# Optimization experiments

Hardware: AMD Instinct MI355X
Metric: run time of the kernel (lower is better)

## Reference

```python
import jax, jax.numpy as jnp
import numpy as np

B, T, I, H, A = 128, 1024, 128, 256, 40


def setup_inputs() -> dict:
    key = jax.random.key(0)
    ks = jax.random.split(key, 10)
    s_ih = 1.0 / np.sqrt(H)
    return {
        "x": jax.random.normal(ks[0], (B, T, I), dtype=jnp.float32),
        "W_ih": jax.random.uniform(ks[1], (3 * H, I), minval=-s_ih, maxval=s_ih, dtype=jnp.float32),
        "W_hh": jax.random.uniform(ks[2], (3 * H, H), minval=-s_ih, maxval=s_ih, dtype=jnp.float32),
        "b_ih": jax.random.uniform(ks[3], (3 * H,), minval=-s_ih, maxval=s_ih, dtype=jnp.float32),
        "b_hh": jax.random.uniform(ks[4], (3 * H,), minval=-s_ih, maxval=s_ih, dtype=jnp.float32),
        "wv_W": jax.random.normal(ks[5], (A, H), dtype=jnp.float32) * 0.05,
        "wv_b": jnp.zeros((A,), dtype=jnp.float32),
        "wu": jax.random.uniform(ks[6], (A,), dtype=jnp.float32),
        "h2o_W": jax.random.normal(ks[7], (1, H), dtype=jnp.float32) * 0.05,
        "h2o_b": jnp.zeros((1,), dtype=jnp.float32),
    }


def _gru_outputs(x, W_ih, W_hh, b_ih, b_hh):
    # Precompute input-side gate projections for all timesteps: [B,T,3H]
    gx = jnp.einsum("bti,gi->btg", x, W_ih) + b_ih
    h0 = jnp.zeros((x.shape[0], H), dtype=x.dtype)

    def step(h, gx_t):
        gh = h @ W_hh.T + b_hh                      # [B,3H]
        xr, xz, xn = jnp.split(gx_t, 3, axis=-1)    # torch gate order r,z,n
        hr, hz, hn = jnp.split(gh, 3, axis=-1)
        r = jax.nn.sigmoid(xr + hr)
        z = jax.nn.sigmoid(xz + hz)
        n = jnp.tanh(xn + r * hn)
        h_new = (1.0 - z) * n + z * h
        return h_new, h_new

    _, hs = jax.lax.scan(step, h0, jnp.swapaxes(gx, 0, 1))  # hs: [T,B,H]
    return jnp.swapaxes(hs, 0, 1)  # [B,T,H]


def reference(x, W_ih, W_hh, b_ih, b_hh, wv_W, wv_b, wu, h2o_W, h2o_b):
    outputs = _gru_outputs(x, W_ih, W_hh, b_ih, b_hh)          # [B,T,H]
    um = jnp.tanh(jnp.einsum("bth,ah->bta", outputs, wv_W) + wv_b)  # [B,T,A]
    alpha = jax.nn.softmax(um @ wu, axis=1)                    # [B,T]
    context = jnp.einsum("bt,bth->bh", alpha, outputs)         # [B,H]
    # dropout_layer is identity in eval mode
    out = context @ h2o_W.T + h2o_b                            # [B,1]
    return out
```

## Files before the change

### kernel.cpp

```cpp
#include <hip/hip_runtime.h>


#define B_ 128
#define T_ 1024
#define I_ 128
#define H_ 256
#define G_ 768
#define A_ 40

typedef _Float16 f16;
typedef _Float16 f16x2 __attribute__((ext_vector_type(2)));
typedef _Float16 f16x8 __attribute__((ext_vector_type(8)));
typedef float    f32x4 __attribute__((ext_vector_type(4)));

__device__ __forceinline__ float fdot2(unsigned a, unsigned b, float c){
#if __has_builtin(__builtin_amdgcn_fdot2)
  return __builtin_amdgcn_fdot2(__builtin_bit_cast(f16x2, a),
                                __builtin_bit_cast(f16x2, b), c, false);
#else
  f16x2 av = __builtin_bit_cast(f16x2, a), bv = __builtin_bit_cast(f16x2, b);
  return c + (float)av.x * (float)bv.x + (float)av.y * (float)bv.y;
#endif
}

__device__ __forceinline__ float2 h2f(unsigned u){
  f16x2 h = __builtin_bit_cast(f16x2, u);
  return make_float2((float)h.x, (float)h.y);
}
__device__ __forceinline__ unsigned f2h2(float a, float b){
  f16x2 h; h.x = (f16)a; h.y = (f16)b;
  return __builtin_bit_cast(unsigned, h);
}
__device__ __forceinline__ float rcp_(float x){ return __builtin_amdgcn_rcpf(x); }
__device__ __forceinline__ float sigm_(float x){ return rcp_(1.f + __expf(-x)); }
__device__ __forceinline__ float tanh_(float x){ return 1.f - 2.f * rcp_(__expf(2.f * x) + 1.f); }

__device__ __forceinline__ float pl16_sum(float x){
  float y = x;
  asm volatile("v_permlane16_swap_b32 %0, %1" : "+v"(x), "+v"(y));
  return x + y;
}
__device__ __forceinline__ float pl32_sum(float x){
  float y = x;
  asm volatile("v_permlane32_swap_b32 %0, %1" : "+v"(x), "+v"(y));
  return x + y;
}

__global__ __launch_bounds__(256) void k_prep_w(const float* __restrict__ W,
                                                unsigned* __restrict__ Wp){
  int idx = blockIdx.x * 256 + threadIdx.x;
  int dd  = idx >> 10;
  int col = idx & 1023;
  int c = dd >> 5, d = dd & 31;
  int rt = ((col >> 6) << 4) | (col & 15);
  int qs = (col >> 4) & 3;
  int r = c * 256 + rt;
  int k = qs * 64 + 2 * d;
  Wp[(size_t)dd * 1024 + col] = f2h2(W[r * 256 + k], W[r * 256 + k + 1]);
}

__global__ __launch_bounds__(256) void k_gx(const float* __restrict__ x,
                                            const float* __restrict__ wih,
                                            const float* __restrict__ bih,
                                            const float* __restrict__ bhh,
                                            f16* __restrict__ gx){
  __shared__ __align__(16) f16 XA[128 * 128];
  __shared__ __align__(16) f16 XB[64 * 128];
  const int tid = threadIdx.x;
  const int m0 = blockIdx.x * 128, n0 = blockIdx.y * 64;

  #pragma unroll
  for (int u = 0; u < 16; ++u){
    int idx = tid + 256 * u;
    int row = idx >> 5, k4 = idx & 31;
    float4 v = *(const float4*)(x + (size_t)(m0 + row) * I_ + k4 * 4);
    unsigned byte = (unsigned)(row * 256 + k4 * 8) ^ ((row & 7) << 4);
    *(uint2*)((char*)XA + byte) = make_uint2(f2h2(v.x, v.y), f2h2(v.z, v.w));
  }
  #pragma unroll
  for (int u = 0; u < 8; ++u){
    int idx = tid + 256 * u;
    int row = idx >> 5, k4 = idx & 31;
    float4 v = *(const float4*)(wih + (size_t)(n0 + row) * I_ + k4 * 4);
    unsigned byte = (unsigned)(row * 256 + k4 * 8) ^ ((row & 7) << 4);
    *(uint2*)((char*)XB + byte) = make_uint2(f2h2(v.x, v.y), f2h2(v.z, v.w));
  }
  __syncthreads();

  const int l = tid & 63, w = tid >> 6;
  const int q = l >> 4, m16 = l & 15;
  f32x4 acc[2][4];
  #pragma unroll
  for (int i = 0; i < 2; ++i)
    #pragma unroll
    for (int nt = 0; nt < 4; ++nt) acc[i][nt] = (f32x4){0.f, 0.f, 0.f, 0.f};

  #pragma unroll
  for (int kt = 0; kt < 4; ++kt){
    f16x8 af[2];
    #pragma unroll
    for (int i = 0; i < 2; ++i){
      int row = (2 * w + i) * 16 + m16;
      unsigned byte = (unsigned)(row * 256 + kt * 64 + q * 16) ^ ((row & 7) << 4);
      af[i] = *(const f16x8*)((const char*)XA + byte);
    }
    #pragma unroll
    for (int nt = 0; nt < 4; ++nt){
      int row = nt * 16 + m16;
      unsigned byte = (unsigned)(row * 256 + kt * 64 + q * 16) ^ ((row & 7) << 4);
      f16x8 bv = *(const f16x8*)((const char*)XB + byte);
      acc[0][nt] = __builtin_amdgcn_mfma_f32_16x16x32_f16(af[0], bv, acc[0][nt], 0, 0, 0);
      acc[1][nt] = __builtin_amdgcn_mfma_f32_16x16x32_f16(af[1], bv, acc[1][nt], 0, 0, 0);
    }
  }

  float bn[4];
  #pragma unroll
  for (int nt = 0; nt < 4; ++nt){
    int n = n0 + nt * 16 + m16;
    bn[nt] = bih[n] + (n < 512 ? bhh[n] : 0.f);
  }

  __syncthreads();
  f16* ST = XA;
  #pragma unroll
  for (int i = 0; i < 2; ++i)
    #pragma unroll
    for (int nt = 0; nt < 4; ++nt)
      #pragma unroll
      for (int j = 0; j < 4; ++j){
        int row = (2 * w + i) * 16 + 4 * q + j;
        ST[row * 72 + nt * 16 + m16] = (f16)(acc[i][nt][j] + bn[nt]);
      }
  __syncthreads();
  #pragma unroll
  for (int u = 0; u < 4; ++u){
    int idx = tid + 256 * u;
    int row = idx >> 3, c = idx & 7;
    uint4 v = *(const uint4*)(ST + row * 72 + c * 8);
    *(uint4*)(gx + (size_t)(m0 + row) * G_ + n0 + c * 8) = v;
  }
}

__global__ __launch_bounds__(1024, 4) void k_gru(const unsigned* __restrict__ Wp,
                                                 unsigned* __restrict__ gx,
                                                 const float* __restrict__ bhh){
  __shared__ uint4 hb[2][4][9];
  const int tid = threadIdx.x;
  const int w = tid >> 6, l = tid & 63;
  const int rt = (w << 4) | (l & 15);
  const int qs = l >> 4;
  const int b = blockIdx.x;

  unsigned w0[32], w1[32], w2[32];
  #pragma unroll
  for (int d = 0; d < 32; ++d) w0[d] = Wp[(size_t)(d     ) * 1024 + tid];
  #pragma unroll
  for (int d = 0; d < 32; ++d) w1[d] = Wp[(size_t)(32 + d) * 1024 + tid];
  #pragma unroll
  for (int d = 0; d < 32; ++d) w2[d] = Wp[(size_t)(64 + d) * 1024 + tid];

  const float bn_ = bhh[512 + rt];
  float hprev = 0.f;
  if (tid < 72) ((uint4*)hb)[tid] = make_uint4(0, 0, 0, 0);

  f16* gxp = (f16*)gx + (size_t)b * T_ * G_;

  f16 xr0 = gxp[rt],      xz0 = gxp[H_ + rt],      xn0 = gxp[2 * H_ + rt];
  f16 xr1 = gxp[G_ + rt], xz1 = gxp[G_ + H_ + rt], xn1 = gxp[G_ + 2 * H_ + rt];
  __syncthreads();

  int cur = 0;
  for (int t = 0; t < T_; ++t){
    const f16* nx = gxp + (size_t)((t + 2) & (T_ - 1)) * G_;
    f16 xr2 = nx[rt], xz2 = nx[H_ + rt], xn2 = nx[2 * H_ + rt];

    float a0 = 0.f, b0 = 0.f, a1 = 0.f, b1 = 0.f, a2 = 0.f, b2 = 0.f;
    #pragma unroll
    for (int i = 0; i < 8; ++i){
      uint4 hv = hb[cur][qs][i];
      a0 = fdot2(w0[4*i+0], hv.x, a0); b0 = fdot2(w0[4*i+1], hv.y, b0);
      a0 = fdot2(w0[4*i+2], hv.z, a0); b0 = fdot2(w0[4*i+3], hv.w, b0);
      a1 = fdot2(w1[4*i+0], hv.x, a1); b1 = fdot2(w1[4*i+1], hv.y, b1);
      a1 = fdot2(w1[4*i+2], hv.z, a1); b1 = fdot2(w1[4*i+3], hv.w, b1);
      a2 = fdot2(w2[4*i+0], hv.x, a2); b2 = fdot2(w2[4*i+1], hv.y, b2);
      a2 = fdot2(w2[4*i+2], hv.z, a2); b2 = fdot2(w2[4*i+3], hv.w, b2);
    }
    float ar = pl32_sum(pl16_sum(a0 + b0));
    float az = pl32_sum(pl16_sum(a1 + b1));
    float an = pl32_sum(pl16_sum(a2 + b2));

    float rg = sigm_((float)xr0 + ar);
    float zg = sigm_((float)xz0 + az);
    float ng = tanh_((float)xn0 + rg * (an + bn_));
    float h  = (1.f - zg) * ng + zg * hprev;
    hprev = h;
    if (qs == 0){
      f16 hh = (f16)h;
      ((f16*)&hb[cur ^ 1][rt >> 6][0])[rt & 63] = hh;
      gxp[(size_t)t * G_ + rt] = hh;
    }
    xr0 = xr1; xz0 = xz1; xn0 = xn1;
    xr1 = xr2; xz1 = xz2; xn1 = xn2;

    asm volatile("s_waitcnt lgkmcnt(0)" ::: "memory");
    __builtin_amdgcn_s_barrier();
    asm volatile("" ::: "memory");
    cur ^= 1;
  }
}

__global__ __launch_bounds__(256) void k_score(const f16* __restrict__ outs,
                                               const float* __restrict__ wvW,
                                               const float* __restrict__ wvb,
                                               const float* __restrict__ wu,
                                               float* __restrict__ s){
  __shared__ uint4 OT[32 * 33];
  __shared__ float WV[A_ * 260];
  const int tid = threadIdx.x;
  const int m0 = blockIdx.x * 32;

  #pragma unroll
  for (int u = 0; u < 4; ++u){
    int idx = tid + 256 * u;
    int row = idx >> 5, col = idx & 31;
    OT[row * 33 + col] = *(const uint4*)(outs + (size_t)(m0 + row) * G_ + col * 8);
  }
  #pragma unroll
  for (int u = 0; u < 10; ++u){
    int f = tid + 256 * u;
    int a = f >> 6, k4 = f & 63;
    float4 v = *(const float4*)(wvW + a * 256 + k4 * 4);
    *(float4*)(WV + a * 260 + k4 * 4) = v;
  }
  __syncthreads();

  const int m = tid >> 3, aq = tid & 7;
  float acc[5] = {0.f, 0.f, 0.f, 0.f, 0.f};
  for (int i = 0; i < 32; ++i){
    uint4 oc = OT[m * 33 + i];
    float2 o01 = h2f(oc.x), o23 = h2f(oc.y), o45 = h2f(oc.z), o67 = h2f(oc.w);
    #pragma unroll
    for (int sa = 0; sa < 5; ++sa){
      int a = aq + sa * 8;
      const float* wr = &WV[a * 260 + i * 8];
      float4 w0 = *(const float4*)wr;
      float4 w1 = *(const float4*)(wr + 4);
      acc[sa] += o01.x*w0.x + o01.y*w0.y + o23.x*w0.z + o23.y*w0.w
               + o45.x*w1.x + o45.y*w1.y + o67.x*w1.z + o67.y*w1.w;
    }
  }
  float sp = 0.f;
  #pragma unroll
  for (int sa = 0; sa < 5; ++sa){
    int a = aq + sa * 8;
    sp += wu[a] * tanh_(acc[sa] + wvb[a]);
  }
  sp += __shfl_xor(sp, 1);
  sp += __shfl_xor(sp, 2);
  sp += __shfl_xor(sp, 4);
  if (aq == 0) s[m0 + m] = sp;
}

__global__ __launch_bounds__(256) void k_ctx(const f16* __restrict__ outs,
                                             const float* __restrict__ s,
                                             const float* __restrict__ h2oW,
                                             const float* __restrict__ h2ob,
                                             float* __restrict__ out){
  __shared__ float AL[T_];
  __shared__ float red[8];
  const int tid = threadIdx.x;
  const int b = blockIdx.x;
  const float* sb = s + (size_t)b * T_;

  float v0 = sb[tid], v1 = sb[tid + 256], v2 = sb[tid + 512], v3 = sb[tid + 768];
  float mx = fmaxf(fmaxf(v0, v1), fmaxf(v2, v3));
  #pragma unroll
  for (int msk = 1; msk < 64; msk <<= 1) mx = fmaxf(mx, __shfl_xor(mx, msk));
  if ((tid & 63) == 0) red[tid >> 6] = mx;
  __syncthreads();
  mx = fmaxf(fmaxf(red[0], red[1]), fmaxf(red[2], red[3]));

  float e0 = __expf(v0 - mx), e1 = __expf(v1 - mx), e2 = __expf(v2 - mx), e3 = __expf(v3 - mx);
  float zs = e0 + e1 + e2 + e3;
  #pragma unroll
  for (int msk = 1; msk < 64; msk <<= 1) zs += __shfl_xor(zs, msk);
  if ((tid & 63) == 0) red[4 + (tid >> 6)] = zs;
  __syncthreads();
  float invZ = 1.f / (red[4] + red[5] + red[6] + red[7]);
  AL[tid] = e0 * invZ; AL[tid + 256] = e1 * invZ;
  AL[tid + 512] = e2 * invZ; AL[tid + 768] = e3 * invZ;
  __syncthreads();

  const f16* ob = outs + (size_t)b * T_ * G_;
  float acc = 0.f;
  for (int t = 0; t < T_; t += 4){
    acc += AL[t + 0] * (float)ob[(size_t)(t + 0) * G_ + tid];
    acc += AL[t + 1] * (float)ob[(size_t)(t + 1) * G_ + tid];
    acc += AL[t + 2] * (float)ob[(size_t)(t + 2) * G_ + tid];
    acc += AL[t + 3] * (float)ob[(size_t)(t + 3) * G_ + tid];
  }
  __syncthreads();
  float val = acc * h2oW[tid];
  #pragma unroll
  for (int msk = 1; msk < 64; msk <<= 1) val += __shfl_xor(val, msk);
  if ((tid & 63) == 0) red[tid >> 6] = val;
  __syncthreads();
  if (tid == 0) out[b] = red[0] + red[1] + red[2] + red[3] + h2ob[0];
}

extern "C" void kernel_launch(void* const* d_in, const int* in_sizes, int n_in,
                              void* d_out, int out_size, void* d_ws, size_t ws_size,
                              hipStream_t stream){
  const float* x    = (const float*)d_in[0];
  const float* wih  = (const float*)d_in[1];
  const float* whh  = (const float*)d_in[2];
  const float* bih  = (const float*)d_in[3];
  const float* bhh  = (const float*)d_in[4];
  const float* wvW  = (const float*)d_in[5];
  const float* wvb  = (const float*)d_in[6];
  const float* wu   = (const float*)d_in[7];
  const float* h2oW = (const float*)d_in[8];
  const float* h2ob = (const float*)d_in[9];
  float* out = (float*)d_out;

  char* ws = (char*)d_ws;
  float*    s  = (float*)ws;
  unsigned* Wp = (unsigned*)(ws + 524288);
  unsigned* gx = (unsigned*)(ws + 917504);

  k_prep_w<<<384, 256, 0, stream>>>(whh, Wp);
  k_gx<<<dim3((B_ * T_) / 128, G_ / 64), 256, 0, stream>>>(x, wih, bih, bhh, (f16*)gx);
  k_gru<<<B_, 1024, 0, stream>>>(Wp, gx, bhh);
  k_score<<<(B_ * T_) / 32, 256, 0, stream>>>((const f16*)gx, wvW, wvb, wu, s);
  k_ctx<<<B_, 256, 0, stream>>>((const f16*)gx, s, h2oW, h2ob, out);
}
```

Measured before the change: 1.749 ms.

## Remap GRU recurrence to 512 threads with 4 rows per thread and DPP reductions

The recurrent kernel now uses 512 threads per batch block instead of 1024. Each group of 8 lanes owns 4 hidden units across all three gates, splitting K into 8 slices of 32 and holding 192 packed fp16 weight registers per thread. Cross-lane reductions over the 8 K-slices use DPP and ds_swizzle instead of permlane swaps, and the hidden-state buffer is padded to avoid bank conflicts. This is meant to cut barrier participants and per-step overhead, at the cost of higher register pressure and only one lane in eight doing the gate math.

```diff
diff --git a/kernel.cpp b/kernel.cpp
--- a/kernel.cpp
+++ b/kernel.cpp
@@ -35,28 +35,22 @@
 __device__ __forceinline__ float sigm_(float x){ return rcp_(1.f + __expf(-x)); }
 __device__ __forceinline__ float tanh_(float x){ return 1.f - 2.f * rcp_(__expf(2.f * x) + 1.f); }
 
-__device__ __forceinline__ float pl16_sum(float x){
-  float y = x;
-  asm volatile("v_permlane16_swap_b32 %0, %1" : "+v"(x), "+v"(y));
-  return x + y;
-}
-__device__ __forceinline__ float pl32_sum(float x){
-  float y = x;
-  asm volatile("v_permlane32_swap_b32 %0, %1" : "+v"(x), "+v"(y));
-  return x + y;
+template<int PAT>
+__device__ __forceinline__ float dppf(float x){
+  return __builtin_bit_cast(float,
+      __builtin_amdgcn_update_dpp(0, __builtin_bit_cast(int, x), PAT, 0xF, 0xF, true));
 }
 
 __global__ __launch_bounds__(256) void k_prep_w(const float* __restrict__ W,
                                                 unsigned* __restrict__ Wp){
   int idx = blockIdx.x * 256 + threadIdx.x;
-  int dd  = idx >> 10;
-  int col = idx & 1023;
-  int c = dd >> 5, d = dd & 31;
-  int rt = ((col >> 6) << 4) | (col & 15);
-  int qs = (col >> 4) & 3;
-  int r = c * 256 + rt;
-  int k = qs * 64 + 2 * d;
-  Wp[(size_t)dd * 1024 + col] = f2h2(W[r * 256 + k], W[r * 256 + k + 1]);
+  int dd  = idx >> 9;
+  int col = idx & 511;
+  int c = dd >> 6, j = (dd >> 4) & 3, d = dd & 15;
+  int rg = col >> 3, ks = col & 7;
+  int row = 256 * c + 4 * rg + j;
+  int k = 32 * ks + 2 * d;
+  Wp[(size_t)dd * 512 + col] = f2h2(W[row * 256 + k], W[row * 256 + k + 1]);
 }
 
 __global__ __launch_bounds__(256) void k_gx(const float* __restrict__ x,
@@ -142,66 +136,101 @@
   }
 }
 
-__global__ __launch_bounds__(1024, 4) void k_gru(const unsigned* __restrict__ Wp,
-                                                 unsigned* __restrict__ gx,
-                                                 const float* __restrict__ bhh){
-  __shared__ uint4 hb[2][4][9];
+__global__ __launch_bounds__(512, 2) void k_gru(const unsigned* __restrict__ Wp,
+                                                unsigned* __restrict__ gx,
+                                                const float* __restrict__ bhh){
+  __shared__ __align__(16) unsigned hb[2][160];
   const int tid = threadIdx.x;
-  const int w = tid >> 6, l = tid & 63;
-  const int rt = (w << 4) | (l & 15);
-  const int qs = l >> 4;
+  const int rg = tid >> 3, ks = tid & 7;
   const int b = blockIdx.x;
 
-  unsigned w0[32], w1[32], w2[32];
-  #pragma unroll
-  for (int d = 0; d < 32; ++d) w0[d] = Wp[(size_t)(d     ) * 1024 + tid];
-  #pragma unroll
-  for (int d = 0; d < 32; ++d) w1[d] = Wp[(size_t)(32 + d) * 1024 + tid];
-  #pragma unroll
-  for (int d = 0; d < 32; ++d) w2[d] = Wp[(size_t)(64 + d) * 1024 + tid];
-
-  const float bn_ = bhh[512 + rt];
-  float hprev = 0.f;
-  if (tid < 72) ((uint4*)hb)[tid] = make_uint4(0, 0, 0, 0);
+  unsigned w[192];
+  #pragma unroll
+  for (int d = 0; d < 192; ++d) w[d] = Wp[(size_t)d * 512 + tid];
+
+  float bn[4];
+  #pragma unroll
+  for (int j = 0; j < 4; ++j) bn[j] = bhh[512 + 4 * rg + j];
+
+  float hprev[4] = {0.f, 0.f, 0.f, 0.f};
+  if (tid < 160){ hb[0][tid] = 0u; }
 
   f16* gxp = (f16*)gx + (size_t)b * T_ * G_;
 
-  f16 xr0 = gxp[rt],      xz0 = gxp[H_ + rt],      xn0 = gxp[2 * H_ + rt];
-  f16 xr1 = gxp[G_ + rt], xz1 = gxp[G_ + H_ + rt], xn1 = gxp[G_ + 2 * H_ + rt];
-  __syncthreads();
-
+  uint2 xr0 = {0,0}, xz0 = {0,0}, xn0 = {0,0};
+  uint2 xr1 = {0,0}, xz1 = {0,0}, xn1 = {0,0};
+  if (ks == 0){
+    xr0 = *(const uint2*)(gxp + 4 * rg);
+    xz0 = *(const uint2*)(gxp + 256 + 4 * rg);
+    xn0 = *(const uint2*)(gxp + 512 + 4 * rg);
+    xr1 = *(const uint2*)(gxp + G_ + 4 * rg);
+    xz1 = *(const uint2*)(gxp + G_ + 256 + 4 * rg);
+    xn1 = *(const uint2*)(gxp + G_ + 512 + 4 * rg);
+  }
+  __syncthreads();
+
+  const int rbase = 20 * ks;
+  const int wdw = 2 * rg + 4 * (rg >> 3);
   int cur = 0;
   for (int t = 0; t < T_; ++t){
-    const f16* nx = gxp + (size_t)((t + 2) & (T_ - 1)) * G_;
-    f16 xr2 = nx[rt], xz2 = nx[H_ + rt], xn2 = nx[2 * H_ + rt];
-
-    float a0 = 0.f, b0 = 0.f, a1 = 0.f, b1 = 0.f, a2 = 0.f, b2 = 0.f;
-    #pragma unroll
-    for (int i = 0; i < 8; ++i){
-      uint4 hv = hb[cur][qs][i];
-      a0 = fdot2(w0[4*i+0], hv.x, a0); b0 = fdot2(w0[4*i+1], hv.y, b0);
-      a0 = fdot2(w0[4*i+2], hv.z, a0); b0 = fdot2(w0[4*i+3], hv.w, b0);
-      a1 = fdot2(w1[4*i+0], hv.x, a1); b1 = fdot2(w1[4*i+1], hv.y, b1);
-      a1 = fdot2(w1[4*i+2], hv.z, a1); b1 = fdot2(w1[4*i+3], hv.w, b1);
-      a2 = fdot2(w2[4*i+0], hv.x, a2); b2 = fdot2(w2[4*i+1], hv.y, b2);
-      a2 = fdot2(w2[4*i+2], hv.z, a2); b2 = fdot2(w2[4*i+3], hv.w, b2);
-    }
-    float ar = pl32_sum(pl16_sum(a0 + b0));
-    float az = pl32_sum(pl16_sum(a1 + b1));
-    float an = pl32_sum(pl16_sum(a2 + b2));
-
-    float rg = sigm_((float)xr0 + ar);
-    float zg = sigm_((float)xz0 + az);
-    float ng = tanh_((float)xn0 + rg * (an + bn_));
-    float h  = (1.f - zg) * ng + zg * hprev;
-    hprev = h;
-    if (qs == 0){
-      f16 hh = (f16)h;
-      ((f16*)&hb[cur ^ 1][rt >> 6][0])[rt & 63] = hh;
-      gxp[(size_t)t * G_ + rt] = hh;
-    }
-    xr0 = xr1; xz0 = xz1; xn0 = xn1;
-    xr1 = xr2; xz1 = xz2; xn1 = xn2;
+    uint4 h0 = *(const uint4*)&hb[cur][rbase + 0];
+    uint4 h1 = *(const uint4*)&hb[cur][rbase + 4];
+    uint4 h2 = *(const uint4*)&hb[cur][rbase + 8];
+    uint4 h3 = *(const uint4*)&hb[cur][rbase + 12];
+
+    float s[12];
+    #pragma unroll
+    for (int q = 0; q < 12; ++q) s[q] = 0.f;
+    #pragma unroll
+    for (int q = 0; q < 12; ++q){
+      const unsigned* wq = &w[q * 16];
+      s[q] = fdot2(wq[0],  h0.x, s[q]); s[q] = fdot2(wq[1],  h0.y, s[q]);
+      s[q] = fdot2(wq[2],  h0.z, s[q]); s[q] = fdot2(wq[3],  h0.w, s[q]);
+      s[q] = fdot2(wq[4],  h1.x, s[q]); s[q] = fdot2(wq[5],  h1.y, s[q]);
+      s[q] = fdot2(wq[6],  h1.z, s[q]); s[q] = fdot2(wq[7],  h1.w, s[q]);
+      s[q] = fdot2(wq[8],  h2.x, s[q]); s[q] = fdot2(wq[9],  h2.y, s[q]);
+      s[q] = fdot2(wq[10], h2.z, s[q]); s[q] = fdot2(wq[11], h2.w, s[q]);
+      s[q] = fdot2(wq[12], h3.x, s[q]); s[q] = fdot2(wq[13], h3.y, s[q]);
+      s[q] = fdot2(wq[14], h3.z, s[q]); s[q] = fdot2(wq[15], h3.w, s[q]);
+    }
+    #pragma unroll
+    for (int q = 0; q < 12; ++q){
+      float x = s[q];
+      x += dppf<0xB1>(x);
+      x += dppf<0x4E>(x);
+      x += __builtin_bit_cast(float,
+            __builtin_amdgcn_ds_swizzle(__builtin_bit_cast(int, x), 0x101F));
+      s[q] = x;
+    }
+
+    if (ks == 0){
+      const f16* nx = gxp + (size_t)((t + 2) & (T_ - 1)) * G_;
+      uint2 xr2 = *(const uint2*)(nx + 4 * rg);
+      uint2 xz2 = *(const uint2*)(nx + 256 + 4 * rg);
+      uint2 xn2 = *(const uint2*)(nx + 512 + 4 * rg);
+
+      float2 ra = h2f(xr0.x), rb = h2f(xr0.y);
+      float2 za = h2f(xz0.x), zb = h2f(xz0.y);
+      float2 na = h2f(xn0.x), nb = h2f(xn0.y);
+      float xrj[4] = {ra.x, ra.y, rb.x, rb.y};
+      float xzj[4] = {za.x, za.y, zb.x, zb.y};
+      float xnj[4] = {na.x, na.y, nb.x, nb.y};
+      float hh[4];
+      #pragma unroll
+      for (int j = 0; j < 4; ++j){
+        float r = sigm_(xrj[j] + s[j]);
+        float z = sigm_(xzj[j] + s[4 + j]);
+        float n = tanh_(xnj[j] + r * (s[8 + j] + bn[j]));
+        float h = (1.f - z) * n + z * hprev[j];
+        hprev[j] = h;
+        hh[j] = h;
+      }
+      uint2 hw = make_uint2(f2h2(hh[0], hh[1]), f2h2(hh[2], hh[3]));
+      *(uint2*)&hb[cur ^ 1][wdw] = hw;
+      *(uint2*)(gxp + (size_t)t * G_ + 4 * rg) = hw;
+      xr0 = xr1; xz0 = xz1; xn0 = xn1;
+      xr1 = xr2; xz1 = xz2; xn1 = xn2;
+    }
 
     asm volatile("s_waitcnt lgkmcnt(0)" ::: "memory");
     __builtin_amdgcn_s_barrier();
@@ -331,7 +360,7 @@
 
   k_prep_w<<<384, 256, 0, stream>>>(whh, Wp);
   k_gx<<<dim3((B_ * T_) / 128, G_ / 64), 256, 0, stream>>>(x, wih, bih, bhh, (f16*)gx);
-  k_gru<<<B_, 1024, 0, stream>>>(Wp, gx, bhh);
+  k_gru<<<B_, 512, 0, stream>>>(Wp, gx, bhh);
   k_score<<<(B_ * T_) / 32, 256, 0, stream>>>((const f16*)gx, wvW, wvb, wu, s);
   k_ctx<<<B_, 256, 0, stream>>>((const f16*)gx, s, h2oW, h2ob, out);
 }
```

After: 1.822 ms. 1.04x slower.
